# Kernel optimization log

Hardware: AMD Instinct MI355X
Metric: run time of the kernel (lower is better)

Reference implementation:

```python
import jax, jax.numpy as jnp
import numpy as np

B, T, U = 4, 256, 64
D_ENC, D_DEC, V = 512, 512, 1024
IN_F = D_ENC + D_DEC  # 1024


def setup_inputs() -> dict:
    key = jax.random.key(0)
    ks = jax.random.split(key, 10)
    enc = jax.random.normal(ks[0], (B, T, D_ENC), dtype=jnp.float32)
    dec = jax.random.normal(ks[1], (B, U, D_DEC), dtype=jnp.float32)
    # ragged lengths in [len/2, len]; force max to be attained so padded
    # shape equals the torch packed output shape (MaxPad == (T, U)).
    enc_lens = jax.random.randint(ks[2], (B,), T // 2, T + 1, dtype=jnp.int32).at[0].set(T)
    dec_lens = jax.random.randint(ks[3], (B,), U // 2, U + 1, dtype=jnp.int32).at[0].set(U)
    s_e = 1.0 / np.sqrt(D_ENC)
    s_d = 1.0 / np.sqrt(D_DEC)
    s_f = 1.0 / np.sqrt(IN_F)
    W_enc = jax.random.uniform(ks[4], (D_ENC, IN_F), jnp.float32, -s_e, s_e)
    b_enc = jax.random.uniform(ks[5], (IN_F,), jnp.float32, -s_e, s_e)
    W_dec = jax.random.uniform(ks[6], (D_DEC, IN_F), jnp.float32, -s_d, s_d)
    b_dec = jax.random.uniform(ks[7], (IN_F,), jnp.float32, -s_d, s_d)
    W_fc = jax.random.uniform(ks[8], (IN_F, V), jnp.float32, -s_f, s_f)
    b_fc = jax.random.uniform(ks[9], (V,), jnp.float32, -s_f, s_f)
    return dict(enc=enc, dec=dec, W_enc=W_enc, b_enc=b_enc, W_dec=W_dec,
                b_dec=b_dec, W_fc=W_fc, b_fc=b_fc,
                enc_lens=enc_lens, dec_lens=dec_lens)


def reference(enc, dec, W_enc, b_enc, W_dec, b_dec, W_fc, b_fc, enc_lens, dec_lens):
    # per-frame / per-label projections: [B,T,IN_F], [B,U,IN_F]
    pe = jnp.einsum('btd,df->btf', enc, W_enc) + b_enc
    pd = jnp.einsum('bud,df->buf', dec, W_dec) + b_dec
    # broadcast-add joint grid: [B,T,U,IN_F]
    h = pe[:, :, None, :] + pd[:, None, :, :]
    logits = jnp.einsum('btuf,fv->btuv', jnp.tanh(h), W_fc) + b_fc
    logp = jax.nn.log_softmax(logits, axis=-1)
    # zero out cells beyond (enc_len_b, dec_len_b), matching F.pad(value=0.)
    t_ok = jnp.arange(T)[None, :] < enc_lens[:, None]          # [B,T]
    u_ok = jnp.arange(U)[None, :] < dec_lens[:, None]          # [B,U]
    mask = (t_ok[:, :, None] & u_ok[:, None, :])[..., None]    # [B,T,U,1]
    return jnp.where(mask, logp, 0.0)
```

## Files before the change

kernel.cpp:

```cpp
#include <hip/hip_runtime.h>
#include <hip/hip_bf16.h>


#define TT 256
#define UU 64
#define VV 1024
#define FF 1024
#define DK 512

typedef __bf16 bf16x8 __attribute__((ext_vector_type(8)));
typedef float  f32x16 __attribute__((ext_vector_type(16)));

__device__ __forceinline__ float fast_tanh(float x) {
  float ax = __builtin_fabsf(x);
  float e  = __expf(-2.0f * ax);
  float r  = (1.0f - e) * __builtin_amdgcn_rcpf(1.0f + e);
  return __builtin_copysignf(r, x);
}

__global__ __launch_bounds__(256)
void pack_w(const float* __restrict__ Wfc, const float* __restrict__ Wenc,
            const float* __restrict__ Wdec,
            __bf16* __restrict__ Pfc, __bf16* __restrict__ Pen, __bf16* __restrict__ Pde)
{
  int bi = blockIdx.x;
  const float* W; __bf16* P; int base;
  if (bi < 512)      { W = Wfc;  P = Pfc; base = bi; }
  else if (bi < 768) { W = Wenc; P = Pen; base = bi - 512; }
  else               { W = Wdec; P = Pde; base = bi - 768; }
  int idx = base * 256 + threadIdx.x;
  int k8 = idx >> 10, v = idx & 1023;
  bf16x8 o;
#pragma unroll
  for (int j = 0; j < 8; ++j) o[j] = (__bf16)W[(k8 * 8 + j) * 1024 + v];
  *(bf16x8*)(P + (size_t)idx * 8) = o;
}

__global__ __launch_bounds__(256)
void proj_mfma(const float* __restrict__ enc, const float* __restrict__ dec,
               const __bf16* __restrict__ Pen, const __bf16* __restrict__ Pde,
               const float* __restrict__ be, const float* __restrict__ bd,
               float* __restrict__ pe, float* __restrict__ pd)
{
  constexpr int BK = 128;
  __shared__ __align__(16) char As[2][64 * BK * 2];
  const int tid = threadIdx.x;
  const int lane = tid & 63;
  const int wid  = tid >> 6;
  const int l31  = lane & 31;
  const int lhi  = lane >> 5;

  int bi = blockIdx.x;
  const float* X; const __bf16* PW; const float* bias; float* P; int rt, ct;
  if (bi < 64) { X = enc; PW = Pen; bias = be; P = pe; rt = bi >> 2; ct = bi & 3; }
  else { int bj = bi - 64; X = dec; PW = Pde; bias = bd; P = pd; rt = bj >> 2; ct = bj & 3; }
  const int r0 = rt * 64;

  auto fillA = [&](int buf, int kc) {
#pragma unroll
    for (int i = 0; i < 4; ++i) {
      int tau = i * 256 + tid;
      int r = tau >> 4, g = tau & 15;
      int k = kc * BK + g * 8;
      const float4* x4 = (const float4*)(X + (r0 + r) * DK + k);
      float4 a0 = x4[0], a1 = x4[1];
      float xv[8] = {a0.x, a0.y, a0.z, a0.w, a1.x, a1.y, a1.z, a1.w};
      bf16x8 p;
#pragma unroll
      for (int q = 0; q < 8; ++q) p[q] = (__bf16)xv[q];
      *(bf16x8*)(&As[buf][r * (BK * 2) + ((g * 16) ^ ((r & 7) << 4))]) = p;
    }
  };

  f32x16 acc[2][2];
#pragma unroll
  for (int mi = 0; mi < 2; ++mi)
#pragma unroll
    for (int ni = 0; ni < 2; ++ni)
#pragma unroll
      for (int q = 0; q < 16; ++q) acc[mi][ni][q] = 0.f;

  fillA(0, 0);
  __syncthreads();
  const int colBase = ct * 256 + wid * 64 + l31;
  for (int kc = 0; kc < DK / BK; ++kc) {
    if (kc + 1 < DK / BK) fillA((kc + 1) & 1, kc + 1);
    const char* Ab = As[kc & 1];
#pragma unroll 2
    for (int ks = 0; ks < BK / 16; ++ks) {
      int k8 = (kc * 8 + ks) * 2 + lhi;
      bf16x8 bfr[2];
#pragma unroll
      for (int ni = 0; ni < 2; ++ni)
        bfr[ni] = *(const bf16x8*)(PW + ((size_t)k8 * VV + colBase + ni * 32) * 8);
      bf16x8 afr[2];
#pragma unroll
      for (int mi = 0; mi < 2; ++mi) {
        int ra = mi * 32 + l31;
        int kb = ks * 32 + lhi * 16;
        afr[mi] = *(const bf16x8*)(&Ab[ra * (BK * 2) + (kb ^ ((ra & 7) << 4))]);
      }
#pragma unroll
      for (int mi = 0; mi < 2; ++mi)
#pragma unroll
        for (int ni = 0; ni < 2; ++ni)
          acc[mi][ni] = __builtin_amdgcn_mfma_f32_32x32x16_bf16(afr[mi], bfr[ni], acc[mi][ni], 0, 0, 0);
    }
    __syncthreads();
  }
  float bv[2];
#pragma unroll
  for (int ni = 0; ni < 2; ++ni) bv[ni] = bias[colBase + ni * 32];
#pragma unroll
  for (int mi = 0; mi < 2; ++mi)
#pragma unroll
    for (int j = 0; j < 16; ++j) {
      int row = r0 + mi * 32 + (j & 3) + 8 * (j >> 2) + 4 * lhi;
#pragma unroll
      for (int ni = 0; ni < 2; ++ni)
        P[row * VV + colBase + ni * 32] = acc[mi][ni][j] + bv[ni];
    }
}

__global__ __launch_bounds__(512, 2)
void joint_main(const float* __restrict__ pe, const float* __restrict__ pd,
                const __bf16* __restrict__ pW, const float* __restrict__ bfc,
                const int* __restrict__ elens, const int* __restrict__ dlens,
                float* __restrict__ out)
{
  __shared__ __align__(16) unsigned char Bb[2][65536];
  __shared__ __align__(16) unsigned char Ab[2][8192];
  __shared__ float pr[8][64];
  __shared__ float lseS[64];

  const int blk = blockIdx.x;
  const int b = blk >> 8;
  const int t = blk & 255;
  const int tid = threadIdx.x;
  const int elen = elens[b], dlen = dlens[b];
  float* outBase = out + (size_t)blk * (UU * VV);

  if (t >= elen) {
    float4 z = {0.f, 0.f, 0.f, 0.f};
#pragma unroll 4
    for (int i = tid; i < UU * VV / 4; i += 512) ((float4*)outBase)[i] = z;
    return;
  }

  const int lane = tid & 63;
  const int wid  = tid >> 6;
  const int l31  = lane & 31;
  const int lhi  = lane >> 5;
  const int colLane = wid * 128 + l31;

  const float* peRow  = pe + (size_t)blk * FF;
  const float* pdBase = pd + (size_t)b * UU * FF;

  auto stageB = [&](int kc, int bi) {
    const __bf16* gp0 = pW + (size_t)kc * 32768;
#pragma unroll
    for (int i = 0; i < 8; ++i) {
      int fbase = i * 512 + wid * 64;
      __builtin_amdgcn_global_load_lds(
        (const __attribute__((address_space(1))) void*)(gp0 + ((size_t)(fbase + lane)) * 8),
        (__attribute__((address_space(3))) void*)(&Bb[bi][fbase * 16]),
        16, 0, 0);
    }
  };

  float4 R0, R1, R2, R3;
  const int ar = tid >> 3;
  const int akg = tid & 7;
  auto issueA = [&](int s) {
    int k = s * 64 + akg * 8;
    const float4* e4 = (const float4*)(peRow + k);
    const float4* d4 = (const float4*)(pdBase + (size_t)ar * FF + k);
    R0 = e4[0]; R1 = e4[1]; R2 = d4[0]; R3 = d4[1];
  };
  auto commitA = [&](int s) {
    float hv[8] = {R0.x + R2.x, R0.y + R2.y, R0.z + R2.z, R0.w + R2.w,
                   R1.x + R3.x, R1.y + R3.y, R1.z + R3.z, R1.w + R3.w};
    bf16x8 p;
#pragma unroll
    for (int e = 0; e < 8; ++e) p[e] = (__bf16)fast_tanh(hv[e]);
    *(bf16x8*)(&Ab[s & 1][ar * 128 + ((akg ^ (ar & 7)) << 4)]) = p;
  };

  f32x16 acc[2][4];
#pragma unroll
  for (int mi = 0; mi < 2; ++mi)
#pragma unroll
    for (int ni = 0; ni < 4; ++ni)
#pragma unroll
      for (int q = 0; q < 16; ++q) acc[mi][ni][q] = 0.f;

  auto mstep = [&](const unsigned char* Bbuf, const unsigned char* Abuf, int kc, int j) {
    bf16x8 bfr[4];
    const int k8l = 2 * j + lhi;
#pragma unroll
    for (int ni = 0; ni < 4; ++ni)
      bfr[ni] = *(const bf16x8*)(Bbuf + ((size_t)((k8l << 10) + colLane + (ni << 5)) << 4));
    bf16x8 afr[2];
    const int kg = ((kc & 1) << 2) + (j << 1) + lhi;
#pragma unroll
    for (int mi = 0; mi < 2; ++mi) {
      int row = mi * 32 + l31;
      afr[mi] = *(const bf16x8*)(Abuf + row * 128 + ((kg ^ (row & 7)) << 4));
    }
#pragma unroll
    for (int mi = 0; mi < 2; ++mi)
#pragma unroll
      for (int ni = 0; ni < 4; ++ni)
        acc[mi][ni] = __builtin_amdgcn_mfma_f32_32x32x16_bf16(afr[mi], bfr[ni], acc[mi][ni], 0, 0, 0);
  };

  issueA(0);
  commitA(0);
  stageB(0, 0);
  issueA(1);
  asm volatile("s_waitcnt vmcnt(4)" ::: "memory");
  asm volatile("s_waitcnt lgkmcnt(0)" ::: "memory");
  __builtin_amdgcn_sched_barrier(0);
  __builtin_amdgcn_s_barrier();
  __builtin_amdgcn_sched_barrier(0);

  for (int kc = 0; kc < 32; ++kc) {
    if (kc < 31) stageB(kc + 1, (kc + 1) & 1);
    if (kc >= 2 && (kc & 1) == 0 && (kc / 2 + 1) <= 15) issueA(kc / 2 + 1);
    __builtin_amdgcn_sched_barrier(0);
    const unsigned char* Bbuf = Bb[kc & 1];
    const unsigned char* Abuf = Ab[(kc >> 1) & 1];
    __builtin_amdgcn_s_setprio(1);
    mstep(Bbuf, Abuf, kc, 0);
    mstep(Bbuf, Abuf, kc, 1);
    __builtin_amdgcn_s_setprio(0);
    if ((kc & 1) == 1 && ((kc + 1) / 2) <= 15) commitA((kc + 1) / 2);
    if (kc < 31) {
      asm volatile("s_waitcnt vmcnt(0)" ::: "memory");
      asm volatile("s_waitcnt lgkmcnt(0)" ::: "memory");
      __builtin_amdgcn_sched_barrier(0);
      __builtin_amdgcn_s_barrier();
      __builtin_amdgcn_sched_barrier(0);
    }
  }

  float bias[4];
#pragma unroll
  for (int ni = 0; ni < 4; ++ni) bias[ni] = bfc[colLane + ni * 32];

  float rsum[2][16];
#pragma unroll
  for (int mi = 0; mi < 2; ++mi)
#pragma unroll
    for (int j = 0; j < 16; ++j) {
      float s = 0.f;
#pragma unroll
      for (int ni = 0; ni < 4; ++ni) {
        float v = acc[mi][ni][j] + bias[ni];
        acc[mi][ni][j] = v;
        s += __expf(v);
      }
      rsum[mi][j] = s;
    }
#pragma unroll
  for (int s = 1; s < 32; s <<= 1) {
#pragma unroll
    for (int mi = 0; mi < 2; ++mi)
#pragma unroll
      for (int j = 0; j < 16; ++j)
        rsum[mi][j] += __shfl_xor(rsum[mi][j], s, 64);
  }
#pragma unroll
  for (int mi = 0; mi < 2; ++mi)
#pragma unroll
    for (int j = 0; j < 16; ++j)
      if (l31 == j) {
        int row = mi * 32 + (j & 3) + 8 * (j >> 2) + 4 * lhi;
        pr[wid][row] = rsum[mi][j];
      }
  __syncthreads();
  if (tid < 64) {
    float s = 0.f;
#pragma unroll
    for (int w = 0; w < 8; ++w) s += pr[w][tid];
    lseS[tid] = __logf(s);
  }
  __syncthreads();

#pragma unroll
  for (int mi = 0; mi < 2; ++mi)
#pragma unroll
    for (int j = 0; j < 16; ++j) {
      int row = mi * 32 + (j & 3) + 8 * (j >> 2) + 4 * lhi;
      float l = lseS[row];
      bool valid = row < dlen;
#pragma unroll
      for (int ni = 0; ni < 4; ++ni) {
        float v = valid ? (acc[mi][ni][j] - l) : 0.0f;
        outBase[(size_t)row * VV + colLane + ni * 32] = v;
      }
    }
}

extern "C" void kernel_launch(void* const* d_in, const int* in_sizes, int n_in,
                              void* d_out, int out_size, void* d_ws, size_t ws_size,
                              hipStream_t stream)
{
  const float* enc  = (const float*)d_in[0];
  const float* dec  = (const float*)d_in[1];
  const float* Wenc = (const float*)d_in[2];
  const float* benc = (const float*)d_in[3];
  const float* Wdec = (const float*)d_in[4];
  const float* bdec = (const float*)d_in[5];
  const float* Wfc  = (const float*)d_in[6];
  const float* bfc  = (const float*)d_in[7];
  const int* elens  = (const int*)d_in[8];
  const int* dlens  = (const int*)d_in[9];
  float* out = (float*)d_out;

  float* pe = (float*)d_ws;
  float* pd = pe + 1024 * 1024;
  __bf16* Pfc = (__bf16*)(pd + 256 * 1024);
  __bf16* Pen = Pfc + 1024 * 1024;
  __bf16* Pde = Pen + 512 * 1024;

  pack_w<<<1024, 256, 0, stream>>>(Wfc, Wenc, Wdec, Pfc, Pen, Pde);
  proj_mfma<<<80, 256, 0, stream>>>(enc, dec, Pen, Pde, benc, bdec, pe, pd);
  joint_main<<<1024, 512, 0, stream>>>(pe, pd, Pfc, bfc, elens, dlens, out);
}
```

Before: 261.9 us.

## Make B tiles wave-private and cut block barriers to one per A stage

Each wave now stages only the slice of W_fc columns it consumes itself. That lets the B double-buffer be synchronised with per-wave vmcnt waits instead of a workgroup barrier every k-chunk. The loop is unrolled by two k-chunks, so a block barrier is needed only when the tanh A tile is committed, and the final two chunks are peeled. The A tile in LDS moves to a k-major layout with an XOR swizzle on row index. The intent is to cut barrier stalls and let waves drift so their MFMA and load phases overlap. The cost is fragile reliance on manual waitcnt counts and on in-order LDS read-before-write within each wave.

New measurement: 240.4 us. -8.2%, faster.

```diff
diff --git a/kernel.cpp b/kernel.cpp
--- a/kernel.cpp
+++ b/kernel.cpp
@@ -129,7 +129,7 @@
                 float* __restrict__ out)
 {
   __shared__ __align__(16) unsigned char Bb[2][65536];
-  __shared__ __align__(16) unsigned char Ab[2][8192];
+  __shared__ __align__(16) unsigned char Abuf[2][8192];
   __shared__ float pr[8][64];
   __shared__ float lseS[64];
 
@@ -160,16 +160,16 @@
     const __bf16* gp0 = pW + (size_t)kc * 32768;
 #pragma unroll
     for (int i = 0; i < 8; ++i) {
-      int fbase = i * 512 + wid * 64;
+      int fb = (i >> 1) * 1024 + wid * 128 + (i & 1) * 64;
       __builtin_amdgcn_global_load_lds(
-        (const __attribute__((address_space(1))) void*)(gp0 + ((size_t)(fbase + lane)) * 8),
-        (__attribute__((address_space(3))) void*)(&Bb[bi][fbase * 16]),
+        (const __attribute__((address_space(1))) void*)(gp0 + ((size_t)fb + lane) * 8),
+        (__attribute__((address_space(3))) void*)(&Bb[bi][(size_t)fb * 16]),
         16, 0, 0);
     }
   };
 
   float4 R0, R1, R2, R3;
-  const int ar = tid >> 3;
+  const int ar  = tid >> 3;
   const int akg = tid & 7;
   auto issueA = [&](int s) {
     int k = s * 64 + akg * 8;
@@ -183,7 +183,7 @@
     bf16x8 p;
 #pragma unroll
     for (int e = 0; e < 8; ++e) p[e] = (__bf16)fast_tanh(hv[e]);
-    *(bf16x8*)(&Ab[s & 1][ar * 128 + ((akg ^ (ar & 7)) << 4)]) = p;
+    *(bf16x8*)(&Abuf[s & 1][((akg << 6) + (ar ^ akg)) << 4]) = p;
   };
 
   f32x16 acc[2][4];
@@ -194,18 +194,18 @@
 #pragma unroll
       for (int q = 0; q < 16; ++q) acc[mi][ni][q] = 0.f;
 
-  auto mstep = [&](const unsigned char* Bbuf, const unsigned char* Abuf, int kc, int j) {
+  auto mstep = [&](const unsigned char* Bp, const unsigned char* Ap, int kc, int j) {
+    const int k8l = (j << 1) + lhi;
     bf16x8 bfr[4];
-    const int k8l = 2 * j + lhi;
 #pragma unroll
     for (int ni = 0; ni < 4; ++ni)
-      bfr[ni] = *(const bf16x8*)(Bbuf + ((size_t)((k8l << 10) + colLane + (ni << 5)) << 4));
+      bfr[ni] = *(const bf16x8*)(Bp + ((size_t)((k8l << 10) + colLane + (ni << 5)) << 4));
+    const int kg = ((kc & 1) << 2) + (j << 1) + lhi;
     bf16x8 afr[2];
-    const int kg = ((kc & 1) << 2) + (j << 1) + lhi;
 #pragma unroll
     for (int mi = 0; mi < 2; ++mi) {
       int row = mi * 32 + l31;
-      afr[mi] = *(const bf16x8*)(Abuf + row * 128 + ((kg ^ (row & 7)) << 4));
+      afr[mi] = *(const bf16x8*)(Ap + (((kg << 6) + (row ^ kg)) << 4));
     }
 #pragma unroll
     for (int mi = 0; mi < 2; ++mi)
@@ -217,31 +217,49 @@
   issueA(0);
   commitA(0);
   stageB(0, 0);
-  issueA(1);
-  asm volatile("s_waitcnt vmcnt(4)" ::: "memory");
   asm volatile("s_waitcnt lgkmcnt(0)" ::: "memory");
   __builtin_amdgcn_sched_barrier(0);
   __builtin_amdgcn_s_barrier();
   __builtin_amdgcn_sched_barrier(0);
 
-  for (int kc = 0; kc < 32; ++kc) {
-    if (kc < 31) stageB(kc + 1, (kc + 1) & 1);
-    if (kc >= 2 && (kc & 1) == 0 && (kc / 2 + 1) <= 15) issueA(kc / 2 + 1);
-    __builtin_amdgcn_sched_barrier(0);
-    const unsigned char* Bbuf = Bb[kc & 1];
-    const unsigned char* Abuf = Ab[(kc >> 1) & 1];
+#pragma unroll 1
+  for (int s = 0; s < 15; ++s) {
+    const int kc0 = 2 * s;
+    stageB(kc0 + 1, 1);
+    issueA(s + 1);
+    asm volatile("s_waitcnt vmcnt(12)" ::: "memory");
+    __builtin_amdgcn_sched_barrier(0);
     __builtin_amdgcn_s_setprio(1);
-    mstep(Bbuf, Abuf, kc, 0);
-    mstep(Bbuf, Abuf, kc, 1);
+    mstep(Bb[0], Abuf[s & 1], kc0, 0);
+    mstep(Bb[0], Abuf[s & 1], kc0, 1);
     __builtin_amdgcn_s_setprio(0);
-    if ((kc & 1) == 1 && ((kc + 1) / 2) <= 15) commitA((kc + 1) / 2);
-    if (kc < 31) {
-      asm volatile("s_waitcnt vmcnt(0)" ::: "memory");
-      asm volatile("s_waitcnt lgkmcnt(0)" ::: "memory");
-      __builtin_amdgcn_sched_barrier(0);
-      __builtin_amdgcn_s_barrier();
-      __builtin_amdgcn_sched_barrier(0);
-    }
+    stageB(kc0 + 2, 0);
+    asm volatile("s_waitcnt vmcnt(12)" ::: "memory");
+    __builtin_amdgcn_sched_barrier(0);
+    __builtin_amdgcn_s_setprio(1);
+    mstep(Bb[1], Abuf[s & 1], kc0 + 1, 0);
+    mstep(Bb[1], Abuf[s & 1], kc0 + 1, 1);
+    __builtin_amdgcn_s_setprio(0);
+    commitA(s + 1);
+    asm volatile("s_waitcnt lgkmcnt(0)" ::: "memory");
+    __builtin_amdgcn_sched_barrier(0);
+    __builtin_amdgcn_s_barrier();
+    __builtin_amdgcn_sched_barrier(0);
+  }
+  {
+    stageB(31, 1);
+    asm volatile("s_waitcnt vmcnt(8)" ::: "memory");
+    __builtin_amdgcn_sched_barrier(0);
+    __builtin_amdgcn_s_setprio(1);
+    mstep(Bb[0], Abuf[1], 30, 0);
+    mstep(Bb[0], Abuf[1], 30, 1);
+    __builtin_amdgcn_s_setprio(0);
+    asm volatile("s_waitcnt vmcnt(0)" ::: "memory");
+    __builtin_amdgcn_sched_barrier(0);
+    __builtin_amdgcn_s_setprio(1);
+    mstep(Bb[1], Abuf[1], 31, 0);
+    mstep(Bb[1], Abuf[1], 31, 1);
+    __builtin_amdgcn_s_setprio(0);
   }
 
   float bias[4];
```

## Quantize joint FC GEMM to int8 MFMA with per-column weight scales

Applied to the files above, without the earlier changes.

Replaces the bf16 joint GEMM with int8: W_fc is quantized per output column with a max-abs scale, and tanh activations are quantized at a fixed scale of 127, then multiplied with i32 32x32x32 int8 MFMA and dequantized in the epilogue. B staging moves to a 4-deep ring buffer with finer vmcnt waits, and A is staged at half the bytes. This halves operand bytes and doubles MFMA throughput per instruction, at the cost of noticeably reduced numerical accuracy in the logits.

New measurement: 232.4 us. 1.13x faster.

```diff
diff --git a/kernel.cpp b/kernel.cpp
--- a/kernel.cpp
+++ b/kernel.cpp
@@ -10,6 +10,8 @@
 
 typedef __bf16 bf16x8 __attribute__((ext_vector_type(8)));
 typedef float  f32x16 __attribute__((ext_vector_type(16)));
+typedef int    i32x4v __attribute__((ext_vector_type(4)));
+typedef int    i32x16 __attribute__((ext_vector_type(16)));
 
 __device__ __forceinline__ float fast_tanh(float x) {
   float ax = __builtin_fabsf(x);
@@ -19,21 +21,57 @@
 }
 
 __global__ __launch_bounds__(256)
-void pack_w(const float* __restrict__ Wfc, const float* __restrict__ Wenc,
-            const float* __restrict__ Wdec,
-            __bf16* __restrict__ Pfc, __bf16* __restrict__ Pen, __bf16* __restrict__ Pde)
+void prep_w(const float* __restrict__ Wenc, const float* __restrict__ Wdec,
+            const float* __restrict__ Wfc,
+            __bf16* __restrict__ Pen, __bf16* __restrict__ Pde,
+            signed char* __restrict__ Pq, float* __restrict__ sc)
 {
   int bi = blockIdx.x;
-  const float* W; __bf16* P; int base;
-  if (bi < 512)      { W = Wfc;  P = Pfc; base = bi; }
-  else if (bi < 768) { W = Wenc; P = Pen; base = bi - 512; }
-  else               { W = Wdec; P = Pde; base = bi - 768; }
-  int idx = base * 256 + threadIdx.x;
-  int k8 = idx >> 10, v = idx & 1023;
-  bf16x8 o;
-#pragma unroll
-  for (int j = 0; j < 8; ++j) o[j] = (__bf16)W[(k8 * 8 + j) * 1024 + v];
-  *(bf16x8*)(P + (size_t)idx * 8) = o;
+  int tid = threadIdx.x;
+  if (bi < 512) {
+    const float* W = (bi < 256) ? Wenc : Wdec;
+    __bf16* P = (bi < 256) ? Pen : Pde;
+    int base = (bi < 256) ? bi : bi - 256;
+    int idx = base * 256 + tid;
+    int k8 = idx >> 10, v = idx & 1023;
+    bf16x8 o;
+#pragma unroll
+    for (int j = 0; j < 8; ++j) o[j] = (__bf16)W[(k8 * 8 + j) * 1024 + v];
+    *(bf16x8*)(P + (size_t)idx * 8) = o;
+    return;
+  }
+  __shared__ float mx[4][64];
+  __shared__ float smax[64];
+  int blk = bi - 512;
+  int p = tid >> 6;
+  int c = tid & 63;
+  int v = blk * 64 + c;
+  float m = 0.f;
+#pragma unroll 8
+  for (int k = p * 256; k < p * 256 + 256; ++k)
+    m = fmaxf(m, __builtin_fabsf(Wfc[k * 1024 + v]));
+  mx[p][c] = m;
+  __syncthreads();
+  float mm = fmaxf(fmaxf(mx[0][c], mx[1][c]), fmaxf(mx[2][c], mx[3][c]));
+  if (p == 0) { smax[c] = mm; sc[v] = (mm > 0.f) ? mm / 127.f : 1.f; }
+  __syncthreads();
+  float si = (smax[c] > 0.f) ? 127.f / smax[c] : 0.f;
+  for (int k16 = p * 16; k16 < p * 16 + 16; ++k16) {
+    unsigned int w[4];
+#pragma unroll
+    for (int g = 0; g < 4; ++g) {
+      unsigned int a = 0;
+#pragma unroll
+      for (int j = 0; j < 4; ++j) {
+        float x = Wfc[(k16 * 16 + g * 4 + j) * 1024 + v];
+        int q = (int)rintf(x * si);
+        q = q > 127 ? 127 : (q < -127 ? -127 : q);
+        a |= (unsigned int)(q & 255) << (8 * j);
+      }
+      w[g] = a;
+    }
+    *(uint4*)(Pq + ((size_t)k16 * 1024 + v) * 16) = make_uint4(w[0], w[1], w[2], w[3]);
+  }
 }
 
 __global__ __launch_bounds__(256)
@@ -124,12 +162,13 @@
 
 __global__ __launch_bounds__(512, 2)
 void joint_main(const float* __restrict__ pe, const float* __restrict__ pd,
-                const __bf16* __restrict__ pW, const float* __restrict__ bfc,
+                const signed char* __restrict__ Pq, const float* __restrict__ sc,
+                const float* __restrict__ bfc,
                 const int* __restrict__ elens, const int* __restrict__ dlens,
                 float* __restrict__ out)
 {
-  __shared__ __align__(16) unsigned char Bb[2][65536];
-  __shared__ __align__(16) unsigned char Ab[2][8192];
+  __shared__ __align__(16) unsigned char Bb[4][32768];
+  __shared__ __align__(16) unsigned char Ab[2][4096];
   __shared__ float pr[8][64];
   __shared__ float lseS[64];
 
@@ -156,87 +195,98 @@
   const float* peRow  = pe + (size_t)blk * FF;
   const float* pdBase = pd + (size_t)b * UU * FF;
 
-  auto stageB = [&](int kc, int bi) {
-    const __bf16* gp0 = pW + (size_t)kc * 32768;
-#pragma unroll
-    for (int i = 0; i < 8; ++i) {
-      int fbase = i * 512 + wid * 64;
+  auto stageB = [&](int kc, int buf) {
+    const signed char* gp = Pq + (size_t)kc * 32768;
+#pragma unroll
+    for (int i = 0; i < 4; ++i) {
+      int fb = (i >> 1) * 1024 + wid * 128 + (i & 1) * 64;
       __builtin_amdgcn_global_load_lds(
-        (const __attribute__((address_space(1))) void*)(gp0 + ((size_t)(fbase + lane)) * 8),
-        (__attribute__((address_space(3))) void*)(&Bb[bi][fbase * 16]),
+        (const __attribute__((address_space(1))) void*)(gp + ((size_t)fb + lane) * 16),
+        (__attribute__((address_space(3))) void*)(&Bb[buf][fb * 16]),
         16, 0, 0);
     }
   };
 
   float4 R0, R1, R2, R3;
   const int ar = tid >> 3;
-  const int akg = tid & 7;
+  const int ah = tid & 7;
   auto issueA = [&](int s) {
-    int k = s * 64 + akg * 8;
+    int k = s * 64 + (ah >> 1) * 16 + (ah & 1) * 8;
     const float4* e4 = (const float4*)(peRow + k);
     const float4* d4 = (const float4*)(pdBase + (size_t)ar * FF + k);
     R0 = e4[0]; R1 = e4[1]; R2 = d4[0]; R3 = d4[1];
   };
-  auto commitA = [&](int s) {
+  auto commitA = [&](int buf) {
     float hv[8] = {R0.x + R2.x, R0.y + R2.y, R0.z + R2.z, R0.w + R2.w,
                    R1.x + R3.x, R1.y + R3.y, R1.z + R3.z, R1.w + R3.w};
-    bf16x8 p;
-#pragma unroll
-    for (int e = 0; e < 8; ++e) p[e] = (__bf16)fast_tanh(hv[e]);
-    *(bf16x8*)(&Ab[s & 1][ar * 128 + ((akg ^ (ar & 7)) << 4)]) = p;
-  };
-
-  f32x16 acc[2][4];
+    unsigned int lo = 0, hi = 0;
+#pragma unroll
+    for (int e = 0; e < 4; ++e) {
+      int q = (int)rintf(fast_tanh(hv[e]) * 127.f);
+      lo |= (unsigned int)(q & 255) << (8 * e);
+    }
+#pragma unroll
+    for (int e = 0; e < 4; ++e) {
+      int q = (int)rintf(fast_tanh(hv[4 + e]) * 127.f);
+      hi |= (unsigned int)(q & 255) << (8 * e);
+    }
+    *(uint2*)(&Ab[buf][(((ah >> 1) << 6) + ar) * 16 + ((ah & 1) << 3)]) =
+        make_uint2(lo, hi);
+  };
+
+  i32x16 acc[2][4];
 #pragma unroll
   for (int mi = 0; mi < 2; ++mi)
 #pragma unroll
     for (int ni = 0; ni < 4; ++ni)
 #pragma unroll
-      for (int q = 0; q < 16; ++q) acc[mi][ni][q] = 0.f;
-
-  auto mstep = [&](const unsigned char* Bbuf, const unsigned char* Abuf, int kc, int j) {
-    bf16x8 bfr[4];
-    const int k8l = 2 * j + lhi;
+      for (int q = 0; q < 16; ++q) acc[mi][ni][q] = 0;
+
+  auto mstep = [&](const unsigned char* Bp, const unsigned char* Ap, int kcL) {
+    i32x4v bfr[4];
 #pragma unroll
     for (int ni = 0; ni < 4; ++ni)
-      bfr[ni] = *(const bf16x8*)(Bbuf + ((size_t)((k8l << 10) + colLane + (ni << 5)) << 4));
-    bf16x8 afr[2];
-    const int kg = ((kc & 1) << 2) + (j << 1) + lhi;
-#pragma unroll
-    for (int mi = 0; mi < 2; ++mi) {
-      int row = mi * 32 + l31;
-      afr[mi] = *(const bf16x8*)(Abuf + row * 128 + ((kg ^ (row & 7)) << 4));
-    }
+      bfr[ni] = *(const i32x4v*)(Bp + ((size_t)(lhi * 1024 + colLane + (ni << 5)) << 4));
+    i32x4v afr[2];
 #pragma unroll
     for (int mi = 0; mi < 2; ++mi)
+      afr[mi] = *(const i32x4v*)(Ap + ((((kcL << 1) + lhi) << 6) + mi * 32 + l31) * 16);
+#pragma unroll
+    for (int mi = 0; mi < 2; ++mi)
 #pragma unroll
       for (int ni = 0; ni < 4; ++ni)
-        acc[mi][ni] = __builtin_amdgcn_mfma_f32_32x32x16_bf16(afr[mi], bfr[ni], acc[mi][ni], 0, 0, 0);
+        acc[mi][ni] = __builtin_amdgcn_mfma_i32_32x32x32_i8(afr[mi], bfr[ni], acc[mi][ni], 0, 0, 0);
   };
 
   issueA(0);
   commitA(0);
-  stageB(0, 0);
-  issueA(1);
-  asm volatile("s_waitcnt vmcnt(4)" ::: "memory");
+  stageB(0, 0); stageB(1, 1); stageB(2, 2);
   asm volatile("s_waitcnt lgkmcnt(0)" ::: "memory");
   __builtin_amdgcn_sched_barrier(0);
   __builtin_amdgcn_s_barrier();
   __builtin_amdgcn_sched_barrier(0);
 
+#pragma unroll
   for (int kc = 0; kc < 32; ++kc) {
-    if (kc < 31) stageB(kc + 1, (kc + 1) & 1);
-    if (kc >= 2 && (kc & 1) == 0 && (kc / 2 + 1) <= 15) issueA(kc / 2 + 1);
+    const int s = kc >> 1;
+    if ((kc & 1) == 0 && s + 1 <= 15) {
+      issueA(s + 1);
+      __builtin_amdgcn_sched_barrier(0);
+    }
+    if (kc + 3 < 32) {
+      stageB(kc + 3, (kc + 3) & 3);
+      __builtin_amdgcn_sched_barrier(0);
+    }
+    if (kc <= 28)      asm volatile("s_waitcnt vmcnt(16)" ::: "memory");
+    else if (kc == 29) asm volatile("s_waitcnt vmcnt(12)" ::: "memory");
+    else if (kc == 30) asm volatile("s_waitcnt vmcnt(4)"  ::: "memory");
+    else               asm volatile("s_waitcnt vmcnt(0)"  ::: "memory");
     __builtin_amdgcn_sched_barrier(0);
-    const unsigned char* Bbuf = Bb[kc & 1];
-    const unsigned char* Abuf = Ab[(kc >> 1) & 1];
     __builtin_amdgcn_s_setprio(1);
-    mstep(Bbuf, Abuf, kc, 0);
-    mstep(Bbuf, Abuf, kc, 1);
+    mstep(Bb[kc & 3], Ab[s & 1], kc & 1);
     __builtin_amdgcn_s_setprio(0);
-    if ((kc & 1) == 1 && ((kc + 1) / 2) <= 15) commitA((kc + 1) / 2);
-    if (kc < 31) {
-      asm volatile("s_waitcnt vmcnt(0)" ::: "memory");
+    if ((kc & 1) == 1 && kc < 31) {
+      commitA((s + 1) & 1);
       asm volatile("s_waitcnt lgkmcnt(0)" ::: "memory");
       __builtin_amdgcn_sched_barrier(0);
       __builtin_amdgcn_s_barrier();
@@ -244,31 +294,34 @@
     }
   }
 
-  float bias[4];
-#pragma unroll
-  for (int ni = 0; ni < 4; ++ni) bias[ni] = bfc[colLane + ni * 32];
+  float bias[4], scl[4];
+#pragma unroll
+  for (int ni = 0; ni < 4; ++ni) {
+    bias[ni] = bfc[colLane + ni * 32];
+    scl[ni]  = sc[colLane + ni * 32] * (1.f / 127.f);
+  }
 
   float rsum[2][16];
 #pragma unroll
   for (int mi = 0; mi < 2; ++mi)
 #pragma unroll
     for (int j = 0; j < 16; ++j) {
-      float s = 0.f;
+      float su = 0.f;
 #pragma unroll
       for (int ni = 0; ni < 4; ++ni) {
-        float v = acc[mi][ni][j] + bias[ni];
-        acc[mi][ni][j] = v;
-        s += __expf(v);
-      }
-      rsum[mi][j] = s;
-    }
-#pragma unroll
-  for (int s = 1; s < 32; s <<= 1) {
+        float v = (float)acc[mi][ni][j] * scl[ni] + bias[ni];
+        acc[mi][ni][j] = __float_as_int(v);
+        su += __expf(v);
+      }
+      rsum[mi][j] = su;
+    }
+#pragma unroll
+  for (int st = 1; st < 32; st <<= 1) {
 #pragma unroll
     for (int mi = 0; mi < 2; ++mi)
 #pragma unroll
       for (int j = 0; j < 16; ++j)
-        rsum[mi][j] += __shfl_xor(rsum[mi][j], s, 64);
+        rsum[mi][j] += __shfl_xor(rsum[mi][j], st, 64);
   }
 #pragma unroll
   for (int mi = 0; mi < 2; ++mi)
@@ -280,10 +333,10 @@
       }
   __syncthreads();
   if (tid < 64) {
-    float s = 0.f;
-#pragma unroll
-    for (int w = 0; w < 8; ++w) s += pr[w][tid];
-    lseS[tid] = __logf(s);
+    float su = 0.f;
+#pragma unroll
+    for (int w = 0; w < 8; ++w) su += pr[w][tid];
+    lseS[tid] = __logf(su);
   }
   __syncthreads();
 
@@ -296,7 +349,7 @@
       bool valid = row < dlen;
 #pragma unroll
       for (int ni = 0; ni < 4; ++ni) {
-        float v = valid ? (acc[mi][ni][j] - l) : 0.0f;
+        float v = valid ? (__int_as_float(acc[mi][ni][j]) - l) : 0.0f;
         outBase[(size_t)row * VV + colLane + ni * 32] = v;
       }
     }
@@ -320,11 +373,12 @@
 
   float* pe = (float*)d_ws;
   float* pd = pe + 1024 * 1024;
-  __bf16* Pfc = (__bf16*)(pd + 256 * 1024);
-  __bf16* Pen = Pfc + 1024 * 1024;
+  __bf16* Pen = (__bf16*)(pd + 256 * 1024);
   __bf16* Pde = Pen + 512 * 1024;
-
-  pack_w<<<1024, 256, 0, stream>>>(Wfc, Wenc, Wdec, Pfc, Pen, Pde);
+  signed char* Pq = (signed char*)(Pde + 512 * 1024);
+  float* sc = (float*)(Pq + 1024 * 1024);
+
+  prep_w<<<528, 256, 0, stream>>>(Wenc, Wdec, Wfc, Pen, Pde, Pq, sc);
   proj_mfma<<<80, 256, 0, stream>>>(enc, dec, Pen, Pde, benc, bdec, pe, pd);
-  joint_main<<<1024, 512, 0, stream>>>(pe, pd, Pfc, bfc, elens, dlens, out);
-}
+  joint_main<<<1024, 512, 0, stream>>>(pe, pd, Pq, sc, bfc, elens, dlens, out);
+}
```
